# Performance work log

Hardware: AMD Instinct MI355X
Metric: run time of the kernel (lower is better)

## Reference

```python
import jax, jax.numpy as jnp
import numpy as np

H = 1024
B_DIM = 64  # bottleneck
EPS = 1e-5

def setup_inputs() -> dict:
    key = jax.random.key(0)
    ks = jax.random.split(key, 5)
    x = jax.random.normal(ks[0], (8, 4096, H), dtype=jnp.float32)
    norm_w = jnp.ones((H,), jnp.float32)
    norm_b = jnp.zeros((H,), jnp.float32)
    # nn.Linear default init ~ U(-1/sqrt(fan_in), 1/sqrt(fan_in))
    lim_d = 1.0 / np.sqrt(H)
    down_w = jax.random.uniform(ks[1], (B_DIM, H), jnp.float32, -lim_d, lim_d)
    down_b = jax.random.uniform(ks[2], (B_DIM,), jnp.float32, -lim_d, lim_d)
    # NOTE: original inits up to zeros; we use small random values so the
    # computation (and gradients) are non-degenerate for kernel testing.
    lim_u = 1.0 / np.sqrt(B_DIM)
    up_w = jax.random.uniform(ks[3], (H, B_DIM), jnp.float32, -lim_u, lim_u)
    up_b = jax.random.uniform(ks[4], (H,), jnp.float32, -lim_u, lim_u)
    return {"x": x, "norm_w": norm_w, "norm_b": norm_b,
            "down_w": down_w, "down_b": down_b, "up_w": up_w, "up_b": up_b}

def reference(x, norm_w, norm_b, down_w, down_b, up_w, up_b):
    # LayerNorm over last dim, eps=1e-5 (PyTorch default)
    mu = jnp.mean(x, axis=-1, keepdims=True)
    var = jnp.mean(jnp.square(x - mu), axis=-1, keepdims=True)
    xn = (x - mu) * jax.lax.rsqrt(var + EPS) * norm_w + norm_b
    # down-proj [B,S,H] @ [H,b] -> [B,S,b]
    h = jnp.einsum('bsh,dh->bsd', xn, down_w) + down_b
    h = jax.nn.gelu(h, approximate=False)  # torch nn.GELU default = exact erf
    # up-proj [B,S,b] @ [b,H] -> [B,S,H], residual add
    out = jnp.einsum('bsd,hd->bsh', h, up_w) + up_b
    return x + out
```

## Files before the change

kernel.cpp:

```cpp
#include <hip/hip_runtime.h>


#define HDIM 1024
#define BDIM 64
#define GPAD 72

using s16x8 = __attribute__((ext_vector_type(8))) short;
using f32x4 = __attribute__((ext_vector_type(4))) float;

__device__ float g_wstat[128];

__device__ __forceinline__ short f2bf(float f) {
  unsigned u = __builtin_bit_cast(unsigned, f);
  u += 0x7fffu + ((u >> 16) & 1u);
  return (short)(u >> 16);
}
__device__ __forceinline__ float bf2f(short s) {
  unsigned u = ((unsigned)(unsigned short)s) << 16;
  return __builtin_bit_cast(float, u);
}

extern "C" __global__ void prep_weights(const float* __restrict__ dw,
                                        const float* __restrict__ uw,
                                        const float* __restrict__ nw,
                                        const float* __restrict__ nb,
                                        const float* __restrict__ db,
                                        short* __restrict__ wsbf) {
  const int b = blockIdx.x;
  if (b < 64) {
    int tid = b * 256 + threadIdx.x;
    if (tid < 8192) {
      int off = tid * 8;
      int k = off & (HDIM - 1);
      f32x4 v0 = *(const f32x4*)(dw + off);
      f32x4 v1 = *(const f32x4*)(dw + off + 4);
      f32x4 g0 = *(const f32x4*)(nw + k);
      f32x4 g1 = *(const f32x4*)(nw + k + 4);
      s16x8 o;
#pragma unroll
      for (int j = 0; j < 4; ++j) {
        o[j]     = f2bf(v0[j] * g0[j]);
        o[j + 4] = f2bf(v1[j] * g1[j]);
      }
      *(s16x8*)(wsbf + tid * 8) = o;
    } else {
      int off = (tid - 8192) * 8;
      f32x4 v0 = *(const f32x4*)(uw + off);
      f32x4 v1 = *(const f32x4*)(uw + off + 4);
      s16x8 o;
#pragma unroll
      for (int j = 0; j < 4; ++j) { o[j] = f2bf(v0[j]); o[j + 4] = f2bf(v1[j]); }
      *(s16x8*)(wsbf + tid * 8) = o;
    }
  } else {
    const int t = threadIdx.x;
    const int n = t >> 2, p = t & 3;
    const float* dwn = dw + n * HDIM;
    float s1 = 0.f, s2 = 0.f;
    for (int j = 0; j < 32; ++j) {
      int k = p * 256 + j * 8;
      f32x4 v0 = *(const f32x4*)(dwn + k);
      f32x4 v1 = *(const f32x4*)(dwn + k + 4);
      f32x4 g0 = *(const f32x4*)(nw + k);
      f32x4 g1 = *(const f32x4*)(nw + k + 4);
      f32x4 b0 = *(const f32x4*)(nb + k);
      f32x4 b1 = *(const f32x4*)(nb + k + 4);
#pragma unroll
      for (int jj = 0; jj < 4; ++jj) {
        s1 += bf2f(f2bf(v0[jj] * g0[jj])) + bf2f(f2bf(v1[jj] * g1[jj]));
        s2 += v0[jj] * b0[jj] + v1[jj] * b1[jj];
      }
    }
    s1 += __shfl_xor(s1, 1); s1 += __shfl_xor(s1, 2);
    s2 += __shfl_xor(s2, 1); s2 += __shfl_xor(s2, 2);
    if (p == 0) {
      g_wstat[n]      = s1;
      g_wstat[64 + n] = db[n] + s2;
    }
  }
}

extern "C" __global__ __launch_bounds__(256, 2)
void adapter_fused(const float* __restrict__ x,
                   const float* __restrict__ ub,
                   const short* __restrict__ dwb,
                   const short* __restrict__ uwb,
                   float* __restrict__ out)
{
  __shared__ __align__(16) short gbf[4][16][GPAD];

  const int t    = threadIdx.x;
  const int w    = t >> 6;
  const int lane = t & 63;
  const int q    = lane >> 4;
  const int c    = lane & 15;
  const size_t rowbase = ((size_t)blockIdx.x * 4 + w) * 16;

  const float* pA  = x   + (rowbase + c) * HDIM + q * 8;
  const short* pB0 = dwb + (size_t)( 0 + c) * HDIM + q * 8;
  const short* pB1 = dwb + (size_t)(16 + c) * HDIM + q * 8;
  const short* pB2 = dwb + (size_t)(32 + c) * HDIM + q * 8;
  const short* pB3 = dwb + (size_t)(48 + c) * HDIM + q * 8;

  f32x4 acc0 = {0.f,0.f,0.f,0.f}, acc1 = acc0, acc2 = acc0, acc3 = acc0;
  float sum = 0.f, ssq = 0.f;

#pragma unroll 4
  for (int ks = 0; ks < 32; ++ks) {
    f32x4 v0 = *(const f32x4*)(pA + ks * 32);
    f32x4 v1 = *(const f32x4*)(pA + ks * 32 + 4);
    s16x8 b0 = *(const s16x8*)(pB0 + ks * 32);
    s16x8 b1 = *(const s16x8*)(pB1 + ks * 32);
    s16x8 b2 = *(const s16x8*)(pB2 + ks * 32);
    s16x8 b3 = *(const s16x8*)(pB3 + ks * 32);
    s16x8 a;
#pragma unroll
    for (int j = 0; j < 4; ++j) {
      float f0 = v0[j]; sum += f0; ssq += f0 * f0; a[j]     = f2bf(f0);
      float f1 = v1[j]; sum += f1; ssq += f1 * f1; a[j + 4] = f2bf(f1);
    }
    acc0 = __builtin_amdgcn_mfma_f32_16x16x32_bf16(a, b0, acc0, 0, 0, 0);
    acc1 = __builtin_amdgcn_mfma_f32_16x16x32_bf16(a, b1, acc1, 0, 0, 0);
    acc2 = __builtin_amdgcn_mfma_f32_16x16x32_bf16(a, b2, acc2, 0, 0, 0);
    acc3 = __builtin_amdgcn_mfma_f32_16x16x32_bf16(a, b3, acc3, 0, 0, 0);
  }

  sum += __shfl_xor(sum, 16); sum += __shfl_xor(sum, 32);
  ssq += __shfl_xor(ssq, 16); ssq += __shfl_xor(ssq, 32);
  const float mu  = sum * (1.0f / HDIM);
  const float var = ssq * (1.0f / HDIM) - mu * mu;
  const float rs  = rsqrtf(var + 1e-5f);

  const float sdw0 = g_wstat[  0 + c], sdw1 = g_wstat[ 16 + c],
              sdw2 = g_wstat[ 32 + c], sdw3 = g_wstat[ 48 + c];
  const float dbv0 = g_wstat[ 64 + c], dbv1 = g_wstat[ 80 + c],
              dbv2 = g_wstat[ 96 + c], dbv3 = g_wstat[112 + c];

#pragma unroll
  for (int i = 0; i < 4; ++i) {
    const int src  = q * 4 + i;
    const float m  = __shfl(mu, src);
    const float rv = __shfl(rs, src);
    float h0 = rv * (acc0[i] - m * sdw0) + dbv0;
    float h1 = rv * (acc1[i] - m * sdw1) + dbv1;
    float h2 = rv * (acc2[i] - m * sdw2) + dbv2;
    float h3 = rv * (acc3[i] - m * sdw3) + dbv3;
    short* grow = &gbf[w][src][c];
    grow[0]  = f2bf(0.5f * h0 * (1.0f + erff(h0 * 0.70710678118654752f)));
    grow[16] = f2bf(0.5f * h1 * (1.0f + erff(h1 * 0.70710678118654752f)));
    grow[32] = f2bf(0.5f * h2 * (1.0f + erff(h2 * 0.70710678118654752f)));
    grow[48] = f2bf(0.5f * h3 * (1.0f + erff(h3 * 0.70710678118654752f)));
  }

  asm volatile("" ::: "memory");

  const s16x8 a0 = *(const s16x8*)&gbf[w][c][q * 8];
  const s16x8 a1 = *(const s16x8*)&gbf[w][c][32 + q * 8];

  const float* xr0 = x + (rowbase + q * 4 + 0) * HDIM + c;
  const float* xr1 = x + (rowbase + q * 4 + 1) * HDIM + c;
  const float* xr2 = x + (rowbase + q * 4 + 2) * HDIM + c;
  const float* xr3 = x + (rowbase + q * 4 + 3) * HDIM + c;
  float* or0 = out + (rowbase + q * 4 + 0) * HDIM + c;
  float* or1 = out + (rowbase + q * 4 + 1) * HDIM + c;
  float* or2 = out + (rowbase + q * 4 + 2) * HDIM + c;
  float* or3 = out + (rowbase + q * 4 + 3) * HDIM + c;
  const short* pu = uwb + (size_t)c * BDIM + q * 8;

#pragma unroll 4
  for (int nt = 0; nt < 64; ++nt) {
    const short* uwrow = pu + (size_t)nt * 16 * BDIM;
    s16x8 b0 = *(const s16x8*)(uwrow);
    s16x8 b1 = *(const s16x8*)(uwrow + 32);
    f32x4 o4 = {0.f,0.f,0.f,0.f};
    o4 = __builtin_amdgcn_mfma_f32_16x16x32_bf16(a0, b0, o4, 0, 0, 0);
    o4 = __builtin_amdgcn_mfma_f32_16x16x32_bf16(a1, b1, o4, 0, 0, 0);
    const float ubv = ub[nt * 16 + c];
    const int co = nt * 16;
    or0[co] = o4[0] + ubv + xr0[co];
    or1[co] = o4[1] + ubv + xr1[co];
    or2[co] = o4[2] + ubv + xr2[co];
    or3[co] = o4[3] + ubv + xr3[co];
  }
}

extern "C" void kernel_launch(void* const* d_in, const int* in_sizes, int n_in,
                              void* d_out, int out_size, void* d_ws, size_t ws_size,
                              hipStream_t stream) {
  const float* x  = (const float*)d_in[0];
  const float* nw = (const float*)d_in[1];
  const float* nb = (const float*)d_in[2];
  const float* dw = (const float*)d_in[3];
  const float* db = (const float*)d_in[4];
  const float* uw = (const float*)d_in[5];
  const float* ub = (const float*)d_in[6];
  float* out = (float*)d_out;

  short* wsbf = (short*)d_ws;
  prep_weights<<<65, 256, 0, stream>>>(dw, uw, nw, nb, db, wsbf);

  const int rows = in_sizes[0] / HDIM;
  const int grid = rows / 64;
  adapter_fused<<<grid, 256, 0, stream>>>(x, ub, wsbf, wsbf + 65536, out);
}
```

Before: 317.2 us.

## Split K across waves with LDS reduction, shrink block to 16 rows

Each block now handles 16 rows, with its four waves each reducing a quarter of the hidden dimension for the down-projection and LayerNorm statistics. Partial accumulators and row sums are combined through shared memory, followed by GELU and a shared bf16 tile. Each wave then computes a quarter of the output columns in the up-projection. This shortens per-wave serial loops and raises the grid size and occupancy target to hide memory latency, at the cost of two block barriers and extra LDS traffic.

```diff
diff --git a/kernel.cpp b/kernel.cpp
--- a/kernel.cpp
+++ b/kernel.cpp
@@ -3,7 +3,6 @@
 
 #define HDIM 1024
 #define BDIM 64
-#define GPAD 72
 
 using s16x8 = __attribute__((ext_vector_type(8))) short;
 using f32x4 = __attribute__((ext_vector_type(4))) float;
@@ -80,33 +79,36 @@
   }
 }
 
-extern "C" __global__ __launch_bounds__(256, 2)
+extern "C" __global__ __launch_bounds__(256, 6)
 void adapter_fused(const float* __restrict__ x,
                    const float* __restrict__ ub,
                    const short* __restrict__ dwb,
                    const short* __restrict__ uwb,
                    float* __restrict__ out)
 {
-  __shared__ __align__(16) short gbf[4][16][GPAD];
+  __shared__ __align__(16) float part[4][64][20];
+  __shared__ float ssum[4][16];
+  __shared__ float sssq[4][16];
+  __shared__ __align__(16) short g[16][72];
 
   const int t    = threadIdx.x;
   const int w    = t >> 6;
   const int lane = t & 63;
   const int q    = lane >> 4;
   const int c    = lane & 15;
-  const size_t rowbase = ((size_t)blockIdx.x * 4 + w) * 16;
-
-  const float* pA  = x   + (rowbase + c) * HDIM + q * 8;
-  const short* pB0 = dwb + (size_t)( 0 + c) * HDIM + q * 8;
-  const short* pB1 = dwb + (size_t)(16 + c) * HDIM + q * 8;
-  const short* pB2 = dwb + (size_t)(32 + c) * HDIM + q * 8;
-  const short* pB3 = dwb + (size_t)(48 + c) * HDIM + q * 8;
+  const size_t rowbase = (size_t)blockIdx.x * 16;
+
+  const float* pA  = x   + (rowbase + c) * HDIM + w * 256 + q * 8;
+  const short* pB0 = dwb + (size_t)( 0 + c) * HDIM + w * 256 + q * 8;
+  const short* pB1 = dwb + (size_t)(16 + c) * HDIM + w * 256 + q * 8;
+  const short* pB2 = dwb + (size_t)(32 + c) * HDIM + w * 256 + q * 8;
+  const short* pB3 = dwb + (size_t)(48 + c) * HDIM + w * 256 + q * 8;
 
   f32x4 acc0 = {0.f,0.f,0.f,0.f}, acc1 = acc0, acc2 = acc0, acc3 = acc0;
   float sum = 0.f, ssq = 0.f;
 
-#pragma unroll 4
-  for (int ks = 0; ks < 32; ++ks) {
+#pragma unroll
+  for (int ks = 0; ks < 8; ++ks) {
     f32x4 v0 = *(const f32x4*)(pA + ks * 32);
     f32x4 v1 = *(const f32x4*)(pA + ks * 32 + 4);
     s16x8 b0 = *(const s16x8*)(pB0 + ks * 32);
@@ -127,55 +129,64 @@
 
   sum += __shfl_xor(sum, 16); sum += __shfl_xor(sum, 32);
   ssq += __shfl_xor(ssq, 16); ssq += __shfl_xor(ssq, 32);
-  const float mu  = sum * (1.0f / HDIM);
-  const float var = ssq * (1.0f / HDIM) - mu * mu;
-  const float rs  = rsqrtf(var + 1e-5f);
-
-  const float sdw0 = g_wstat[  0 + c], sdw1 = g_wstat[ 16 + c],
-              sdw2 = g_wstat[ 32 + c], sdw3 = g_wstat[ 48 + c];
-  const float dbv0 = g_wstat[ 64 + c], dbv1 = g_wstat[ 80 + c],
-              dbv2 = g_wstat[ 96 + c], dbv3 = g_wstat[112 + c];
-
-#pragma unroll
-  for (int i = 0; i < 4; ++i) {
-    const int src  = q * 4 + i;
-    const float m  = __shfl(mu, src);
-    const float rv = __shfl(rs, src);
-    float h0 = rv * (acc0[i] - m * sdw0) + dbv0;
-    float h1 = rv * (acc1[i] - m * sdw1) + dbv1;
-    float h2 = rv * (acc2[i] - m * sdw2) + dbv2;
-    float h3 = rv * (acc3[i] - m * sdw3) + dbv3;
-    short* grow = &gbf[w][src][c];
-    grow[0]  = f2bf(0.5f * h0 * (1.0f + erff(h0 * 0.70710678118654752f)));
-    grow[16] = f2bf(0.5f * h1 * (1.0f + erff(h1 * 0.70710678118654752f)));
-    grow[32] = f2bf(0.5f * h2 * (1.0f + erff(h2 * 0.70710678118654752f)));
-    grow[48] = f2bf(0.5f * h3 * (1.0f + erff(h3 * 0.70710678118654752f)));
-  }
-
-  asm volatile("" ::: "memory");
-
-  const s16x8 a0 = *(const s16x8*)&gbf[w][c][q * 8];
-  const s16x8 a1 = *(const s16x8*)&gbf[w][c][32 + q * 8];
-
-  const float* xr0 = x + (rowbase + q * 4 + 0) * HDIM + c;
-  const float* xr1 = x + (rowbase + q * 4 + 1) * HDIM + c;
-  const float* xr2 = x + (rowbase + q * 4 + 2) * HDIM + c;
-  const float* xr3 = x + (rowbase + q * 4 + 3) * HDIM + c;
-  float* or0 = out + (rowbase + q * 4 + 0) * HDIM + c;
-  float* or1 = out + (rowbase + q * 4 + 1) * HDIM + c;
-  float* or2 = out + (rowbase + q * 4 + 2) * HDIM + c;
-  float* or3 = out + (rowbase + q * 4 + 3) * HDIM + c;
-  const short* pu = uwb + (size_t)c * BDIM + q * 8;
+  if (lane < 16) { ssum[w][c] = sum; sssq[w][c] = ssq; }
+
+  *(f32x4*)&part[w][ 0 + c][q * 4] = acc0;
+  *(f32x4*)&part[w][16 + c][q * 4] = acc1;
+  *(f32x4*)&part[w][32 + c][q * 4] = acc2;
+  *(f32x4*)&part[w][48 + c][q * 4] = acc3;
+
+  __syncthreads();
+
+  {
+    const int n = w * 16 + c;
+    f32x4 p0 = *(const f32x4*)&part[0][n][q * 4];
+    f32x4 p1 = *(const f32x4*)&part[1][n][q * 4];
+    f32x4 p2 = *(const f32x4*)&part[2][n][q * 4];
+    f32x4 p3 = *(const f32x4*)&part[3][n][q * 4];
+    f32x4 h4 = (p0 + p1) + (p2 + p3);
+
+    const int rr = lane & 15;
+    float sT = (ssum[0][rr] + ssum[1][rr]) + (ssum[2][rr] + ssum[3][rr]);
+    float qT = (sssq[0][rr] + sssq[1][rr]) + (sssq[2][rr] + sssq[3][rr]);
+    const float muL = sT * (1.0f / HDIM);
+    const float rsL = rsqrtf(qT * (1.0f / HDIM) - muL * muL + 1e-5f);
+
+    const float sdw = g_wstat[n];
+    const float dbv = g_wstat[64 + n];
+#pragma unroll
+    for (int i = 0; i < 4; ++i) {
+      const float m  = __shfl(muL, q * 4 + i);
+      const float rv = __shfl(rsL, q * 4 + i);
+      float h = rv * (h4[i] - m * sdw) + dbv;
+      g[q * 4 + i][n] = f2bf(0.5f * h * (1.0f + erff(h * 0.70710678118654752f)));
+    }
+  }
+  __syncthreads();
+
+  const s16x8 a0 = *(const s16x8*)&g[c][q * 8];
+  const s16x8 a1 = *(const s16x8*)&g[c][32 + q * 8];
+
+  const float* xr0 = x + (rowbase + q * 4 + 0) * HDIM + w * 256 + c;
+  const float* xr1 = x + (rowbase + q * 4 + 1) * HDIM + w * 256 + c;
+  const float* xr2 = x + (rowbase + q * 4 + 2) * HDIM + w * 256 + c;
+  const float* xr3 = x + (rowbase + q * 4 + 3) * HDIM + w * 256 + c;
+  float* or0 = out + (rowbase + q * 4 + 0) * HDIM + w * 256 + c;
+  float* or1 = out + (rowbase + q * 4 + 1) * HDIM + w * 256 + c;
+  float* or2 = out + (rowbase + q * 4 + 2) * HDIM + w * 256 + c;
+  float* or3 = out + (rowbase + q * 4 + 3) * HDIM + w * 256 + c;
+  const short* pu = uwb + (size_t)(w * 256 + c) * BDIM + q * 8;
+  const float* pub = ub + w * 256 + c;
 
 #pragma unroll 4
-  for (int nt = 0; nt < 64; ++nt) {
+  for (int nt = 0; nt < 16; ++nt) {
     const short* uwrow = pu + (size_t)nt * 16 * BDIM;
     s16x8 b0 = *(const s16x8*)(uwrow);
     s16x8 b1 = *(const s16x8*)(uwrow + 32);
     f32x4 o4 = {0.f,0.f,0.f,0.f};
     o4 = __builtin_amdgcn_mfma_f32_16x16x32_bf16(a0, b0, o4, 0, 0, 0);
     o4 = __builtin_amdgcn_mfma_f32_16x16x32_bf16(a1, b1, o4, 0, 0, 0);
-    const float ubv = ub[nt * 16 + c];
+    const float ubv = pub[nt * 16];
     const int co = nt * 16;
     or0[co] = o4[0] + ubv + xr0[co];
     or1[co] = o4[1] + ubv + xr1[co];
@@ -200,6 +211,6 @@
   prep_weights<<<65, 256, 0, stream>>>(dw, uw, nw, nb, db, wsbf);
 
   const int rows = in_sizes[0] / HDIM;
-  const int grid = rows / 64;
+  const int grid = rows / 16;
   adapter_fused<<<grid, 256, 0, stream>>>(x, ub, wsbf, wsbf + 65536, out);
 }
```

Result: no change. 318.5 us (+0.4%).
